# Performance work log

Hardware: AMD Instinct MI355X
Metric: run time of the kernel (lower is better)

The kernel has to match this reference:

```python
import jax, jax.numpy as jnp
import numpy as np

BT, N, D, HEADS, E = 1024, 64, 256, 4, 512
LRELU_SLOPE = 0.2
EPS = 1e-8


def setup_inputs() -> dict:
    key = jax.random.key(0)
    ks = jax.random.split(key, 8)
    d = D
    return {
        "H": jax.random.normal(ks[0], (BT, N, d), jnp.float32),
        "W_lin": jax.random.normal(ks[1], (d, d), jnp.float32) / np.sqrt(d).astype(np.float32),
        "W_val": jax.random.normal(ks[2], (d, d), jnp.float32) / np.sqrt(d).astype(np.float32),
        "a": jax.random.normal(ks[3], (HEADS, d // HEADS), jnp.float32),
        "W_out": jax.random.normal(ks[4], (d, d), jnp.float32) / np.sqrt(d).astype(np.float32),
        "A0": jax.random.uniform(ks[5], (N, N), jnp.float32),
        "src": jax.random.randint(ks[6], (E,), 0, N, jnp.int32),
        "dst": jax.random.randint(ks[7], (E,), 0, N, jnp.int32),
    }


def reference(H, W_lin, W_val, a, W_out, A0, src, dst):
    bt, n, d = H.shape
    h, dh = a.shape
    # projections (torch Linear: x @ W.T)
    Xq = (H @ W_lin.T).reshape(bt, n, h, dh)   # [BT,N,h,dh]
    Xv = (H @ W_val.T).reshape(bt, n, h, dh)
    # per-edge GATv2 scores: edge e goes dst[e] -> src[e] (src aggregates)
    Qs = Xq[:, src]                            # [BT,E,h,dh] receiving node
    Kt = Xq[:, dst]                            # [BT,E,h,dh] neighbor
    e = jnp.einsum('behd,hd->beh', jax.nn.leaky_relu(Qs + Kt, LRELU_SLOPE), a)
    e = e + jnp.log(A0[src, dst] + EPS)[None, :, None]   # anatomical bias
    # segment softmax over edges sharing the same receiving node (src)
    e_t = e.transpose(1, 0, 2)                 # [E,BT,h]
    m = jax.ops.segment_max(e_t, src, num_segments=n)    # [N,BT,h]
    ex = jnp.exp(e_t - m[src])
    denom = jax.ops.segment_sum(ex, src, num_segments=n)
    attn = ex / denom[src]                     # [E,BT,h]
    # weighted scatter of neighbor values
    Vt = Xv[:, dst].transpose(1, 0, 2, 3)      # [E,BT,h,dh]
    Y = jax.ops.segment_sum(attn[..., None] * Vt, src, num_segments=n)  # [N,BT,h,dh]
    Y = Y.transpose(1, 0, 2, 3).reshape(bt, n, d)
    return Y @ W_out.T
```

## Files before the change

kernel.cpp:

```cpp
#include <hip/hip_runtime.h>
#include <math.h>

#define D_    256
#define NE    512
#define NNODE 64
#define NHEAD 4
#define SLOPE 0.2f
#define BTN   65536

typedef __attribute__((ext_vector_type(4))) float f32x4;
typedef __attribute__((ext_vector_type(8))) _Float16 f16x8;
typedef __attribute__((ext_vector_type(2))) _Float16 f16x2;
typedef __attribute__((ext_vector_type(2))) __fp16   h16x2;
typedef unsigned short u16;

__device__ inline u16 f2h(float x) {
    union { _Float16 h; u16 u; } v; v.h = (_Float16)x; return v.u;
}
__device__ inline float h2f(u16 b) {
    union { u16 u; _Float16 h; } v; v.u = b; return (float)v.h;
}
__device__ inline f16x2 pkrtz(float lo, float hi) {
    h16x2 r = __builtin_amdgcn_cvt_pkrtz(lo, hi);
    f16x2 o; __builtin_memcpy(&o, &r, 4); return o;
}

#define GLD16(g, l) __builtin_amdgcn_global_load_lds( \
    (const __attribute__((address_space(1))) void*)(g), \
    (__attribute__((address_space(3))) void*)(l), 16, 0, 0)

__global__ __launch_bounds__(512) void build_edge(const int* __restrict__ src,
    const int* __restrict__ dst, const float* __restrict__ A0,
    int2* __restrict__ gedge)
{
    const int t = threadIdx.x;
    int s = src[t], d = dst[t];
    float lg = logf(A0[s * NNODE + d] + 1e-8f);
    gedge[t] = make_int2((s << 8) | d, __float_as_int(lg));
}

__global__ __launch_bounds__(256) void prep_hi(const float* __restrict__ s,
    u16* __restrict__ h, int n4)
{
    for (int i = blockIdx.x * 256 + threadIdx.x; i < n4; i += gridDim.x * 256) {
        float4 v = ((const float4*)s)[i];
        ((ushort4*)h)[i] = make_ushort4(f2h(v.x), f2h(v.y), f2h(v.z), f2h(v.w));
    }
}

__global__ __launch_bounds__(256) void prep_w3(const float* __restrict__ w0,
    const float* __restrict__ w1, const float* __restrict__ w2,
    u16* __restrict__ h0, u16* __restrict__ h1, u16* __restrict__ h2)
{
    int sel = blockIdx.x >> 6, b = blockIdx.x & 63;
    const float* s = sel == 0 ? w0 : sel == 1 ? w1 : w2;
    u16* h = sel == 0 ? h0 : sel == 1 ? h1 : h2;
    int i = b * 256 + threadIdx.x;
    float4 v = ((const float4*)s)[i];
    ((ushort4*)h)[i] = make_ushort4(f2h(v.x), f2h(v.y), f2h(v.z), f2h(v.w));
}

template<int OMODE>
__global__ __launch_bounds__(256) void gemm_1p(const u16* __restrict__ A,
    const u16* __restrict__ B, void* __restrict__ Cout)
{
    __shared__ u16 sA[4096], sB[4096];
    __shared__ u16 sT[OMODE >= 2 ? 16384 : 16];
    const int t = threadIdx.x, lane = t & 63, wave = t >> 6;
    const int wm = wave >> 1, wn = wave & 1;
    const int bid = blockIdx.x;
    const int swz = (bid & 7) * 128 + (bid >> 3);
    const int m0 = (swz >> 1) * 128, n0 = (swz & 1) * 128;
    const int fr = lane & 15, kq = (lane >> 4) * 8;

    f32x4 acc[4][4];
    #pragma unroll
    for (int i = 0; i < 4; ++i)
        #pragma unroll
        for (int j = 0; j < 4; ++j) acc[i][j] = 0.f;

    for (int k0 = 0; k0 < D_; k0 += 32) {
        #pragma unroll
        for (int s = 0; s < 2; ++s) {
            const int cb = (s * 4 + wave) * 64;
            const int c  = cb + lane;
            const int row = c >> 2, ks = (c & 3) * 8;
            GLD16(A + (size_t)(m0 + row) * D_ + k0 + ks, sA + cb * 8);
            GLD16(B + (size_t)(n0 + row) * D_ + k0 + ks, sB + cb * 8);
        }
        __syncthreads();

        f16x8 fa[4];
        #pragma unroll
        for (int mi = 0; mi < 4; ++mi)
            fa[mi] = *(const f16x8*)(sA + (wm * 64 + mi * 16 + fr) * 32 + kq);
        #pragma unroll
        for (int ni = 0; ni < 4; ++ni) {
            f16x8 fb = *(const f16x8*)(sB + (wn * 64 + ni * 16 + fr) * 32 + kq);
            #pragma unroll
            for (int mi = 0; mi < 4; ++mi)
                acc[mi][ni] = __builtin_amdgcn_mfma_f32_16x16x32_f16(fa[mi], fb, acc[mi][ni], 0, 0, 0);
        }
        __syncthreads();
    }

    const int fq = (lane >> 4) * 4;
    if (OMODE == 0) {
        #pragma unroll
        for (int mi = 0; mi < 4; ++mi)
            #pragma unroll
            for (int ni = 0; ni < 4; ++ni)
                #pragma unroll
                for (int r = 0; r < 4; ++r) {
                    int m = m0 + wm * 64 + mi * 16 + fq + r;
                    int n = n0 + wn * 64 + ni * 16 + fr;
                    ((float*)Cout)[(size_t)m * D_ + n] = acc[mi][ni][r];
                }
    } else {
        u16* wT = sT + wave * 4096;
        #pragma unroll
        for (int mi = 0; mi < 4; ++mi)
            #pragma unroll
            for (int ni = 0; ni < 4; ++ni) {
                int node0 = mi * 16 + fq;
                int dim   = ni * 16 + fr;
                if (OMODE == 2) {
                    ushort4 v = make_ushort4(f2h(acc[mi][ni][0]), f2h(acc[mi][ni][1]),
                                             f2h(acc[mi][ni][2]), f2h(acc[mi][ni][3]));
                    *(ushort4*)&wT[dim * 64 + (((node0 >> 3) ^ (dim & 7)) << 3) + (node0 & 7)] = v;
                } else {
                    #pragma unroll
                    for (int r = 0; r < 4; ++r) {
                        int node = node0 + r;
                        wT[node * 64 + ((((dim >> 3) ^ (node & 7))) << 3) + (dim & 7)]
                            = f2h(acc[mi][ni][r]);
                    }
                }
            }
        __syncthreads();
        const int btq = (m0 >> 6) + wm;
        const int hq  = (n0 >> 6) + wn;
        u16* gx = (u16*)Cout + ((size_t)btq * NHEAD + hq) * 4096;
        #pragma unroll
        for (int r = 0; r < 8; ++r)
            *(f16x8*)&gx[r * 512 + lane * 8] = *(const f16x8*)&wT[r * 512 + lane * 8];
    }
}

__global__ __launch_bounds__(256, 5) void fused_edge_agg(
    const u16* __restrict__ Xqh, const u16* __restrict__ Xvt,
    const int2* __restrict__ gedge, const float* __restrict__ a,
    u16* __restrict__ Yh)
{
    __shared__ u16   sQ[4096];
    __shared__ float sP[4096];
    __shared__ float sBn[NNODE];
    __shared__ float sLin[NE];
    __shared__ int   sPack[NE];

    const int t = threadIdx.x, lane = t & 63, wave = t >> 6;
    const int fr = lane & 15, qtr = lane >> 4;
    const int bt = blockIdx.x >> 2, h = blockIdx.x & 3;

    const u16* gv = Xvt + ((size_t)bt * NHEAD + h) * 4096;
    f16x8 vf[2][4];
    #pragma unroll
    for (int kk = 0; kk < 2; ++kk) {
        int g = kk * 4 + qtr;
        #pragma unroll
        for (int mi = 0; mi < 4; ++mi) {
            int arow = mi * 16 + fr;
            vf[kk][mi] = *(const f16x8*)&gv[arow * 64 + ((g ^ (arow & 7)) << 3)];
        }
    }
    f16x8 af[2];
    #pragma unroll
    for (int kk = 0; kk < 2; ++kk) {
        const float* ab = a + h * 64 + kk * 32 + qtr * 8;
        float4 a0 = *(const float4*)ab, a1 = *(const float4*)(ab + 4);
        af[kk][0] = (_Float16)(0.4f * a0.x); af[kk][1] = (_Float16)(0.4f * a0.y);
        af[kk][2] = (_Float16)(0.4f * a0.z); af[kk][3] = (_Float16)(0.4f * a0.w);
        af[kk][4] = (_Float16)(0.4f * a1.x); af[kk][5] = (_Float16)(0.4f * a1.y);
        af[kk][6] = (_Float16)(0.4f * a1.z); af[kk][7] = (_Float16)(0.4f * a1.w);
    }

    const u16* gq = Xqh + ((size_t)bt * NHEAD + h) * 4096;
    #pragma unroll
    for (int r = 0; r < 2; ++r) {
        int id = r * 256 + t;
        GLD16(gq + id * 8, (char*)sQ + id * 16);
    }
    #pragma unroll
    for (int i = 0; i < 4; ++i)
        ((float4*)sP)[t + i * 256] = make_float4(0.f, 0.f, 0.f, 0.f);
    __syncthreads();

    {
        int n = t >> 2, qq = t & 3;
        float b = 0.f;
        #pragma unroll
        for (int j = 0; j < 2; ++j) {
            int ck = qq * 2 + j;
            f16x8 qv = *(const f16x8*)&sQ[n * 64 + ((ck ^ (n & 7)) << 3)];
            const float* ab = a + h * 64 + ck * 8;
            float4 a0 = *(const float4*)ab, a1 = *(const float4*)(ab + 4);
            b = fmaf((float)qv[0], a0.x, b); b = fmaf((float)qv[1], a0.y, b);
            b = fmaf((float)qv[2], a0.z, b); b = fmaf((float)qv[3], a0.w, b);
            b = fmaf((float)qv[4], a1.x, b); b = fmaf((float)qv[5], a1.y, b);
            b = fmaf((float)qv[6], a1.z, b); b = fmaf((float)qv[7], a1.w, b);
        }
        b += __shfl_xor(b, 1);
        b += __shfl_xor(b, 2);
        if (qq == 0) sBn[n] = b;
    }
    __syncthreads();

    #pragma unroll
    for (int i = 0; i < 2; ++i) {
        int e = t + i * 256;
        int2 ge = gedge[e];
        int s_ = ge.x >> 8, d_ = ge.x & 255;
        sPack[e] = ge.x;
        sLin[e] = 0.6f * (sBn[s_] + sBn[d_]) + __int_as_float(ge.y);
    }
    __syncthreads();

    const int wbase = wave * 128;
    #pragma unroll
    for (int tt = 0; tt < 8; ++tt) {
        int e = wbase + tt * 16 + fr;
        int pk = sPack[e];
        int s_ = pk >> 8, d_ = pk & 255;
        f32x4 acc = 0.f;
        #pragma unroll
        for (int kk = 0; kk < 2; ++kk) {
            int ck = kk * 4 + qtr;
            f16x8 qs = *(const f16x8*)&sQ[s_ * 64 + ((ck ^ (s_ & 7)) << 3)];
            f16x8 qd = *(const f16x8*)&sQ[d_ * 64 + ((ck ^ (d_ & 7)) << 3)];
            f16x8 x = qs + qd;
            unsigned xu[4];
            __builtin_memcpy(xu, &x, 16);
            xu[0] &= 0x7FFF7FFFu; xu[1] &= 0x7FFF7FFFu;
            xu[2] &= 0x7FFF7FFFu; xu[3] &= 0x7FFF7FFFu;
            f16x8 xa;
            __builtin_memcpy(&xa, xu, 16);
            acc = __builtin_amdgcn_mfma_f32_16x16x32_f16(xa, af[kk], acc, 0, 0, 0);
        }
        int c = lane & 15;
        if (c < 4) {
            float av = c == 0 ? acc[0] : c == 1 ? acc[1] : c == 2 ? acc[2] : acc[3];
            int eg = wbase + tt * 16 + qtr * 4 + c;
            int pk2 = sPack[eg];
            atomicAdd(&sP[(pk2 >> 8) * 64 + (pk2 & 255)], __expf(av + sLin[eg]));
        }
    }
    __syncthreads();

    {
        int s_ = t >> 2, qq = t & 3;
        const float4* row = (const float4*)&sP[s_ * 64 + qq * 16];
        float4 v0 = row[0], v1 = row[1], v2 = row[2], v3 = row[3];
        float part = v0.x + v0.y + v0.z + v0.w + v1.x + v1.y + v1.z + v1.w
                   + v2.x + v2.y + v2.z + v2.w + v3.x + v3.y + v3.z + v3.w;
        part += __shfl_xor(part, 1);
        part += __shfl_xor(part, 2);
        float inv = part > 0.f ? 1.f / part : 0.f;
        f16x2 p0 = pkrtz(v0.x * inv, v0.y * inv), p1 = pkrtz(v0.z * inv, v0.w * inv);
        f16x2 p2 = pkrtz(v1.x * inv, v1.y * inv), p3 = pkrtz(v1.z * inv, v1.w * inv);
        f16x2 p4 = pkrtz(v2.x * inv, v2.y * inv), p5 = pkrtz(v2.z * inv, v2.w * inv);
        f16x2 p6 = pkrtz(v3.x * inv, v3.y * inv), p7 = pkrtz(v3.z * inv, v3.w * inv);
        int c0 = qq * 2, c1 = qq * 2 + 1;
        u16* d0 = &sQ[s_ * 64 + ((c0 ^ (s_ & 7)) << 3)];
        u16* d1 = &sQ[s_ * 64 + ((c1 ^ (s_ & 7)) << 3)];
        ((f16x2*)d0)[0] = p0; ((f16x2*)d0)[1] = p1;
        ((f16x2*)d0)[2] = p2; ((f16x2*)d0)[3] = p3;
        ((f16x2*)d1)[0] = p4; ((f16x2*)d1)[1] = p5;
        ((f16x2*)d1)[2] = p6; ((f16x2*)d1)[3] = p7;
    }
    __syncthreads();

    f32x4 acc[4];
    #pragma unroll
    for (int i = 0; i < 4; ++i) acc[i] = 0.f;
    const int srow = wave * 16 + fr;
    #pragma unroll
    for (int kk = 0; kk < 2; ++kk) {
        int g = kk * 4 + qtr;
        f16x8 fb = *(const f16x8*)&sQ[srow * 64 + ((g ^ (srow & 7)) << 3)];
        #pragma unroll
        for (int mi = 0; mi < 4; ++mi)
            acc[mi] = __builtin_amdgcn_mfma_f32_16x16x32_f16(vf[kk][mi], fb, acc[mi], 0, 0, 0);
    }

    const int node = wave * 16 + fr;
    const int fq = qtr * 4;
    u16* yh = Yh + ((size_t)bt * NNODE + node) * D_ + h * 64;
    #pragma unroll
    for (int mi = 0; mi < 4; ++mi) {
        ushort4 v = make_ushort4(f2h(acc[mi][0]), f2h(acc[mi][1]),
                                 f2h(acc[mi][2]), f2h(acc[mi][3]));
        *(ushort4*)&yh[mi * 16 + fq] = v;
    }
}

extern "C" void kernel_launch(void* const* d_in, const int* in_sizes, int n_in,
                              void* d_out, int out_size, void* d_ws, size_t ws_size,
                              hipStream_t stream)
{
    const float* H     = (const float*)d_in[0];
    const float* W_lin = (const float*)d_in[1];
    const float* W_val = (const float*)d_in[2];
    const float* a     = (const float*)d_in[3];
    const float* W_out = (const float*)d_in[4];
    const float* A0    = (const float*)d_in[5];
    const int*   src   = (const int*)d_in[6];
    const int*   dst   = (const int*)d_in[7];

    const size_t nX = (size_t)BTN * D_;
    u16* Hh  = (u16*)d_ws;
    u16* Xqh = Hh + nX;
    u16* Wlh   = Xqh + nX;
    u16* Wvh   = Wlh + D_ * D_;
    u16* Wouth = Wvh + D_ * D_;
    int2* gedge = (int2*)(Wouth + D_ * D_);
    u16* Yh = Hh;
    if (ws_size < (size_t)134217728) return;

    u16* Xvt = (u16*)d_out;

    build_edge<<<1, 512, 0, stream>>>(src, dst, A0, gedge);
    prep_hi<<<4096, 256, 0, stream>>>(H, Hh, (int)(nX / 4));
    prep_w3<<<192, 256, 0, stream>>>(W_lin, W_val, W_out, Wlh, Wvh, Wouth);

    gemm_1p<3><<<1024, 256, 0, stream>>>(Hh, Wlh, Xqh);
    gemm_1p<2><<<1024, 256, 0, stream>>>(Hh, Wvh, Xvt);

    fused_edge_agg<<<4096, 256, 0, stream>>>(Xqh, Xvt, gedge, a, Yh);

    gemm_1p<0><<<1024, 256, 0, stream>>>(Yh, Wouth, (float*)d_out);
}
```

Baseline: 120.3 us.

## Fuse H fp16 conversion into merged Q/V projection GEMM

Drops the separate pass that converts H to fp16 and makes the projection GEMM read fp32 H directly, converting to fp16 while it fills shared memory. The Q and V projections are merged into one launch over a concatenated 512-wide weight matrix. This removes one full read and write of an fp16 copy of H and one kernel launch. In exchange, each GEMM block now loads fp32 A through plain loads and converts in registers instead of using direct-to-LDS loads, and the fp32 H tile is fetched once by each of the four column blocks.

```diff
diff --git a/kernel.cpp b/kernel.cpp
--- a/kernel.cpp
+++ b/kernel.cpp
@@ -17,9 +17,6 @@
 __device__ inline u16 f2h(float x) {
     union { _Float16 h; u16 u; } v; v.h = (_Float16)x; return v.u;
 }
-__device__ inline float h2f(u16 b) {
-    union { u16 u; _Float16 h; } v; v.u = b; return (float)v.h;
-}
 __device__ inline f16x2 pkrtz(float lo, float hi) {
     h16x2 r = __builtin_amdgcn_cvt_pkrtz(lo, hi);
     f16x2 o; __builtin_memcpy(&o, &r, 4); return o;
@@ -37,15 +34,6 @@
     int s = src[t], d = dst[t];
     float lg = logf(A0[s * NNODE + d] + 1e-8f);
     gedge[t] = make_int2((s << 8) | d, __float_as_int(lg));
-}
-
-__global__ __launch_bounds__(256) void prep_hi(const float* __restrict__ s,
-    u16* __restrict__ h, int n4)
-{
-    for (int i = blockIdx.x * 256 + threadIdx.x; i < n4; i += gridDim.x * 256) {
-        float4 v = ((const float4*)s)[i];
-        ((ushort4*)h)[i] = make_ushort4(f2h(v.x), f2h(v.y), f2h(v.z), f2h(v.w));
-    }
 }
 
 __global__ __launch_bounds__(256) void prep_w3(const float* __restrict__ w0,
@@ -60,12 +48,98 @@
     ((ushort4*)h)[i] = make_ushort4(f2h(v.x), f2h(v.y), f2h(v.z), f2h(v.w));
 }
 
-template<int OMODE>
-__global__ __launch_bounds__(256) void gemm_1p(const u16* __restrict__ A,
-    const u16* __restrict__ B, void* __restrict__ Cout)
+__global__ __launch_bounds__(256) void gemm12(const float* __restrict__ A32,
+    const u16* __restrict__ B, u16* __restrict__ Xqh, u16* __restrict__ Xvt)
+{
+    __shared__ u16 sA[128 * 40];
+    __shared__ u16 sB[4096];
+    __shared__ u16 sT[16384];
+    const int t = threadIdx.x, lane = t & 63, wave = t >> 6;
+    const int wm = wave >> 1, wn = wave & 1;
+    const int bid = blockIdx.x;
+    const int swz = (bid & 7) * 256 + (bid >> 3);
+    const int m0 = (swz >> 2) * 128, nq = swz & 3, n0 = nq * 128;
+    const int fr = lane & 15, kq = (lane >> 4) * 8;
+
+    f32x4 acc[4][4];
+    #pragma unroll
+    for (int i = 0; i < 4; ++i)
+        #pragma unroll
+        for (int j = 0; j < 4; ++j) acc[i][j] = 0.f;
+
+    for (int k0 = 0; k0 < D_; k0 += 32) {
+        #pragma unroll
+        for (int rr = 0; rr < 2; ++rr) {
+            int idx = rr * 256 + t;
+            int row = idx >> 2, c8 = (idx & 3) * 8;
+            const float* ap = A32 + (size_t)(m0 + row) * D_ + k0 + c8;
+            float4 v0 = *(const float4*)ap;
+            float4 v1 = *(const float4*)(ap + 4);
+            f16x8 hv;
+            hv[0] = (_Float16)v0.x; hv[1] = (_Float16)v0.y;
+            hv[2] = (_Float16)v0.z; hv[3] = (_Float16)v0.w;
+            hv[4] = (_Float16)v1.x; hv[5] = (_Float16)v1.y;
+            hv[6] = (_Float16)v1.z; hv[7] = (_Float16)v1.w;
+            *(f16x8*)&sA[row * 40 + c8] = hv;
+        }
+        #pragma unroll
+        for (int s = 0; s < 2; ++s) {
+            const int cb = (s * 4 + wave) * 64;
+            const int c  = cb + lane;
+            const int row = c >> 2, ks = (c & 3) * 8;
+            GLD16(B + (size_t)(n0 + row) * D_ + k0 + ks, sB + cb * 8);
+        }
+        __syncthreads();
+
+        f16x8 fa[4];
+        #pragma unroll
+        for (int mi = 0; mi < 4; ++mi)
+            fa[mi] = *(const f16x8*)(sA + (wm * 64 + mi * 16 + fr) * 40 + kq);
+        #pragma unroll
+        for (int ni = 0; ni < 4; ++ni) {
+            f16x8 fb = *(const f16x8*)(sB + (wn * 64 + ni * 16 + fr) * 32 + kq);
+            #pragma unroll
+            for (int mi = 0; mi < 4; ++mi)
+                acc[mi][ni] = __builtin_amdgcn_mfma_f32_16x16x32_f16(fa[mi], fb, acc[mi][ni], 0, 0, 0);
+        }
+        __syncthreads();
+    }
+
+    const int fq = (lane >> 4) * 4;
+    u16* wT = sT + wave * 4096;
+    const bool isQ = nq < 2;
+    #pragma unroll
+    for (int mi = 0; mi < 4; ++mi)
+        #pragma unroll
+        for (int ni = 0; ni < 4; ++ni) {
+            int node0 = mi * 16 + fq;
+            int dim   = ni * 16 + fr;
+            if (!isQ) {
+                ushort4 v = make_ushort4(f2h(acc[mi][ni][0]), f2h(acc[mi][ni][1]),
+                                         f2h(acc[mi][ni][2]), f2h(acc[mi][ni][3]));
+                *(ushort4*)&wT[dim * 64 + (((node0 >> 3) ^ (dim & 7)) << 3) + (node0 & 7)] = v;
+            } else {
+                #pragma unroll
+                for (int r = 0; r < 4; ++r) {
+                    int node = node0 + r;
+                    wT[node * 64 + ((((dim >> 3) ^ (node & 7))) << 3) + (dim & 7)]
+                        = f2h(acc[mi][ni][r]);
+                }
+            }
+        }
+    __syncthreads();
+    const int btq = (m0 >> 6) + wm;
+    const int hq  = isQ ? (n0 >> 6) + wn : ((n0 - 256) >> 6) + wn;
+    u16* gx = (isQ ? Xqh : Xvt) + ((size_t)btq * NHEAD + hq) * 4096;
+    #pragma unroll
+    for (int r = 0; r < 8; ++r)
+        *(f16x8*)&gx[r * 512 + lane * 8] = *(const f16x8*)&wT[r * 512 + lane * 8];
+}
+
+__global__ __launch_bounds__(256) void gemm3(const u16* __restrict__ A,
+    const u16* __restrict__ B, float* __restrict__ Cout)
 {
     __shared__ u16 sA[4096], sB[4096];
-    __shared__ u16 sT[OMODE >= 2 ? 16384 : 16];
     const int t = threadIdx.x, lane = t & 63, wave = t >> 6;
     const int wm = wave >> 1, wn = wave & 1;
     const int bid = blockIdx.x;
@@ -105,46 +179,16 @@
     }
 
     const int fq = (lane >> 4) * 4;
-    if (OMODE == 0) {
-        #pragma unroll
-        for (int mi = 0; mi < 4; ++mi)
+    #pragma unroll
+    for (int mi = 0; mi < 4; ++mi)
+        #pragma unroll
+        for (int ni = 0; ni < 4; ++ni)
             #pragma unroll
-            for (int ni = 0; ni < 4; ++ni)
-                #pragma unroll
-                for (int r = 0; r < 4; ++r) {
-                    int m = m0 + wm * 64 + mi * 16 + fq + r;
-                    int n = n0 + wn * 64 + ni * 16 + fr;
-                    ((float*)Cout)[(size_t)m * D_ + n] = acc[mi][ni][r];
-                }
-    } else {
-        u16* wT = sT + wave * 4096;
-        #pragma unroll
-        for (int mi = 0; mi < 4; ++mi)
-            #pragma unroll
-            for (int ni = 0; ni < 4; ++ni) {
-                int node0 = mi * 16 + fq;
-                int dim   = ni * 16 + fr;
-                if (OMODE == 2) {
-                    ushort4 v = make_ushort4(f2h(acc[mi][ni][0]), f2h(acc[mi][ni][1]),
-                                             f2h(acc[mi][ni][2]), f2h(acc[mi][ni][3]));
-                    *(ushort4*)&wT[dim * 64 + (((node0 >> 3) ^ (dim & 7)) << 3) + (node0 & 7)] = v;
-                } else {
-                    #pragma unroll
-                    for (int r = 0; r < 4; ++r) {
-                        int node = node0 + r;
-                        wT[node * 64 + ((((dim >> 3) ^ (node & 7))) << 3) + (dim & 7)]
-                            = f2h(acc[mi][ni][r]);
-                    }
-                }
+            for (int r = 0; r < 4; ++r) {
+                int m = m0 + wm * 64 + mi * 16 + fq + r;
+                int n = n0 + wn * 64 + ni * 16 + fr;
+                Cout[(size_t)m * D_ + n] = acc[mi][ni][r];
             }
-        __syncthreads();
-        const int btq = (m0 >> 6) + wm;
-        const int hq  = (n0 >> 6) + wn;
-        u16* gx = (u16*)Cout + ((size_t)btq * NHEAD + hq) * 4096;
-        #pragma unroll
-        for (int r = 0; r < 8; ++r)
-            *(f16x8*)&gx[r * 512 + lane * 8] = *(const f16x8*)&wT[r * 512 + lane * 8];
-    }
 }
 
 __global__ __launch_bounds__(256, 5) void fused_edge_agg(
@@ -317,25 +361,22 @@
     const int*   dst   = (const int*)d_in[7];
 
     const size_t nX = (size_t)BTN * D_;
-    u16* Hh  = (u16*)d_ws;
-    u16* Xqh = Hh + nX;
-    u16* Wlh   = Xqh + nX;
-    u16* Wvh   = Wlh + D_ * D_;
-    u16* Wouth = Wvh + D_ * D_;
+    u16*  Xqh   = (u16*)d_ws;
+    u16*  Yh    = Xqh + nX;
+    u16*  Wqv   = Yh + nX;
+    u16*  Wouth = Wqv + 512 * D_;
     int2* gedge = (int2*)(Wouth + D_ * D_);
-    u16* Yh = Hh;
     if (ws_size < (size_t)134217728) return;
 
     u16* Xvt = (u16*)d_out;
 
     build_edge<<<1, 512, 0, stream>>>(src, dst, A0, gedge);
-    prep_hi<<<4096, 256, 0, stream>>>(H, Hh, (int)(nX / 4));
-    prep_w3<<<192, 256, 0, stream>>>(W_lin, W_val, W_out, Wlh, Wvh, Wouth);
-
-    gemm_1p<3><<<1024, 256, 0, stream>>>(Hh, Wlh, Xqh);
-    gemm_1p<2><<<1024, 256, 0, stream>>>(Hh, Wvh, Xvt);
+    prep_w3<<<192, 256, 0, stream>>>(W_lin, W_val, W_out,
+                                     Wqv, Wqv + D_ * D_, Wouth);
+
+    gemm12<<<2048, 256, 0, stream>>>(H, Wqv, Xqh, Xvt);
 
     fused_edge_agg<<<4096, 256, 0, stream>>>(Xqh, Xvt, gedge, a, Yh);
 
-    gemm_1p<0><<<1024, 256, 0, stream>>>(Yh, Wouth, (float*)d_out);
-}
+    gemm3<<<1024, 256, 0, stream>>>(Yh, Wouth, (float*)d_out);
+}
```

Result: faster. 104.5 us (-13.2%).
